# Kernel optimization log

Hardware: AMD Instinct MI355X
Metric: run time of the kernel (lower is better)

Reference implementation:

```python
import jax, jax.numpy as jnp
import numpy as np

B, S, V, E, R1, R2, L = 16, 128, 32000, 128, 256, 640, 512


def pos_encoding(seq_len, d, n=10000.0):
    # P[k, 2i] = sin(k / n^(2i/d)); P[k, 2i+1] = cos(k / n^(2i/d))
    k = jnp.arange(seq_len, dtype=jnp.float32)[:, None]
    i = jnp.arange(d // 2, dtype=jnp.float32)[None, :]
    ang = k / jnp.power(jnp.float32(n), 2.0 * i / d)
    P = jnp.zeros((seq_len, d), dtype=jnp.float32)
    P = P.at[:, 0::2].set(jnp.sin(ang)).at[:, 1::2].set(jnp.cos(ang))
    return P


def setup_inputs() -> dict:
    key = jax.random.key(0)
    ks = iter(jax.random.split(key, 40))

    def lin(fin, fout):
        W = jax.random.normal(next(ks), (fin, fout), jnp.float32) / np.sqrt(fin)
        b = jax.random.normal(next(ks), (fout,), jnp.float32) * 0.01
        return W, b

    inp = {}
    inp['x'] = jax.random.normal(next(ks), (B, S, V), jnp.float32)
    inp['W_emb'], inp['b_emb'] = lin(V, E)
    inp['W_pos1'], inp['b_pos1'] = lin(2 * E, E)
    inp['W_red'], inp['b_red'] = lin(S * E, R1)
    inp['W_pos2'], inp['b_pos2'] = lin(2 * R1, R1)
    inp['W_red2'], inp['b_red2'] = lin(S * R1, R2)
    inp['W_pos3'], inp['b_pos3'] = lin(2 * R2, R2)
    inp['W_down2'], inp['b_down2'] = lin(R2, L)
    inp['W_flat'], inp['b_flat'] = lin(L * S, L)
    inp['W_d1'], inp['b_d1'] = lin(L, L)
    inp['W_d2'], inp['b_d2'] = lin(L, L)
    inp['W_d3'], inp['b_d3'] = lin(L, L)
    inp['W_p1'], inp['b_p1'] = lin(L, V)
    inp['W_p2'], inp['b_p2'] = lin(L, V)
    return inp


def _square_memory(h):
    # einsum('bij,bkm->bikj') factorizes: out[b,i,k,j] = h[b,i,j] * sum_m h[b,k,m]
    b, s, d = h.shape
    row_sum = h.sum(axis=-1)                       # (B, S)
    q = h[:, :, None, :] * row_sum[:, None, :, None]  # (B, S, S, D)
    return q.reshape(b, s, s * d)


def reference(x, W_emb, b_emb, W_pos1, b_pos1, W_red, b_red, W_pos2, b_pos2,
              W_red2, b_red2, W_pos3, b_pos3, W_down2, b_down2, W_flat, b_flat,
              W_d1, b_d1, W_d2, b_d2, W_d3, b_d3, W_p1, b_p1, W_p2, b_p2):
    relu = jax.nn.relu
    h = relu(x @ W_emb + b_emb)                                  # (B,S,E)
    h = h + relu(pos_encoding(S, 2 * E) @ W_pos1 + b_pos1)
    h = relu(_square_memory(h) @ W_red + b_red)                  # (B,S,R1)
    h = h + relu(pos_encoding(S, 2 * R1) @ W_pos2 + b_pos2)
    h = relu(_square_memory(h) @ W_red2 + b_red2)                # (B,S,R2)
    h = h + relu(pos_encoding(S, 2 * R2) @ W_pos3 + b_pos3)
    h = relu(h @ W_down2 + b_down2)                              # (B,S,L)
    h = relu(h.reshape(h.shape[0], -1) @ W_flat + b_flat)        # (B,L)
    h = relu(h @ W_d1 + b_d1)
    p1 = h @ W_p1 + b_p1
    h = relu(h @ W_d2 + b_d2)
    p2 = h @ W_p2 + b_p2
    h = relu(h @ W_d3 + b_d3)
    p3 = h @ W_p1 + b_p1  # faithful to source: project_1 reused (project_3 unused)
    return p1 + p2 + p3
```

## Files before the change

### kernel.cpp

```cpp
#include <hip/hip_runtime.h>

typedef float  f4   __attribute__((ext_vector_type(4)));
typedef __bf16 bf8_t __attribute__((ext_vector_type(8)));
typedef __bf16 bf4_t __attribute__((ext_vector_type(4)));

__device__ __forceinline__ void glds16(const void* g, void* l) {
    __builtin_amdgcn_global_load_lds(
        (const __attribute__((address_space(1))) void*)g,
        (__attribute__((address_space(3))) void*)l, 16, 0, 0);
}

__global__ __launch_bounds__(256)
void prep_kernel(float* __restrict__ P1, float* __restrict__ P2,
                 float* __restrict__ P3,
                 const float* __restrict__ bp1, const float* __restrict__ bp2,
                 float* __restrict__ bc, float* __restrict__ rs2,
                 const float* __restrict__ Wemb, __bf16* __restrict__ WembT,
                 const float* __restrict__ Wd2, __bf16* __restrict__ Wd2T,
                 const float* __restrict__ Wq1, __bf16* __restrict__ Wq1T,
                 const float* __restrict__ Wq2, __bf16* __restrict__ Wq2T,
                 const float* __restrict__ Wq3, __bf16* __restrict__ Wq3T) {
    const int bid = blockIdx.x;
    const int t = threadIdx.x;
    if (bid < 5280) {
        const float* src; __bf16* dst; int CN, RK, tn, local;
        if (bid < 4000)      { src = Wemb; dst = WembT; RK = 32000; CN = 128; tn = 4;  local = bid; }
        else if (bid < 4320) { src = Wd2;  dst = Wd2T;  RK = 640;   CN = 512; tn = 16; local = bid - 4000; }
        else if (bid < 4352) { src = Wq1;  dst = Wq1T;  RK = 256;   CN = 128; tn = 4;  local = bid - 4320; }
        else if (bid < 4480) { src = Wq2;  dst = Wq2T;  RK = 512;   CN = 256; tn = 8;  local = bid - 4352; }
        else                 { src = Wq3;  dst = Wq3T;  RK = 1280;  CN = 640; tn = 20; local = bid - 4480; }
        const int kt = local / tn, ntl = local - kt * tn;
        const int k0 = kt * 32, n0 = ntl * 32;
        __shared__ float tile[32][33];
        const int r = t >> 3, c4 = (t & 7) * 4;
        const f4 v = *(const f4*)(src + (long)(k0 + r) * CN + n0 + c4);
        tile[r][c4] = v[0]; tile[r][c4 + 1] = v[1];
        tile[r][c4 + 2] = v[2]; tile[r][c4 + 3] = v[3];
        __syncthreads();
        bf4_t o2;
        o2[0] = (__bf16)tile[c4][r];     o2[1] = (__bf16)tile[c4 + 1][r];
        o2[2] = (__bf16)tile[c4 + 2][r]; o2[3] = (__bf16)tile[c4 + 3][r];
        *(bf4_t*)(dst + (long)(n0 + r) * RK + k0 + c4) = o2;
        return;
    }
    int idx = (bid - 5280) * 256 + t;
    const int n1 = 128 * 256, n2 = 128 * 512;
    const int nP = 262144;
    if (idx < nP) {
        float* P; int d, local;
        if (idx < n1)           { P = P1; d = 256;  local = idx; }
        else if (idx < n1 + n2) { P = P2; d = 512;  local = idx - n1; }
        else                    { P = P3; d = 1280; local = idx - n1 - n2; }
        int s = local / d;
        int k = local - s * d;
        int i = k >> 1;
        float ang = (float)s * powf(10000.0f, (-2.0f * (float)i) / (float)d);
        P[local] = (k & 1) ? cosf(ang) : sinf(ang);
    } else if (idx < nP + 32000) {
        int j = idx - nP;
        bc[j] = 2.f * bp1[j] + bp2[j];
    } else if (idx < nP + 32000 + 2048) {
        rs2[idx - nP - 32000] = 0.f;
    }
}

template<int BMODE>
__device__ __forceinline__ void gemm_dev(
    float* As0, float* As1, float* Bb0, float* Bb1,
    const float* __restrict__ A, const void* __restrict__ Bv,
    const void* __restrict__ B2v, float* __restrict__ C,
    const float* __restrict__ bias, const float* __restrict__ addsrc,
    float* __restrict__ rsum,
    int M, int N, int K, int lda, int ldb, int ldc, int kswitch,
    long sA, long sB, long sC, int ksplit, int kchunk, int relu,
    int bn, int bm, int bz) {

    const int t = threadIdx.x;
    const int batch = bz / ksplit;
    const int kz = bz - batch * ksplit;
    const int m0 = bm * 64, n0 = bn * 128;
    const int kb = kz * kchunk;
    const int ke = (kb + kchunk < K) ? (kb + kchunk) : K;
    const int nit = (ke - kb + 31) >> 5;

    const int lane = t & 63;
    const int w = t >> 6;
    const int wm = w >> 1, wn = w & 1;
    const int fr = lane & 15;
    const int fq = (lane >> 4) * 8;

    f4 acc[2][4];
#pragma unroll
    for (int mt = 0; mt < 2; ++mt)
#pragma unroll
        for (int nt = 0; nt < 4; ++nt) acc[mt][nt] = (f4){0.f, 0.f, 0.f, 0.f};

    const float* Ab = A + (long)batch * sA;
    const int mvalid = M - m0;

    const int ra = t >> 3;
    const int ja = (t & 7) ^ (ra & 7);
    const float* aS0 = Ab + (long)(m0 + ra) * lda + 4 * ja;
    const float* aS1 = aS0 + 32L * lda;

    const __bf16* bTS0 = nullptr; const __bf16* bTS1 = nullptr;
    const float* bNS0 = nullptr; const float* bNS2 = nullptr;
    if constexpr (BMODE == 0) {
        const __bf16* BT = (const __bf16*)Bv + (long)batch * sB;
        const int nb = t >> 2;
        const int fb = (nb & 3) ^ ((nb >> 2) & 3);
        const int jb = (t & 3) ^ fb;
        bTS0 = BT + (long)(n0 + nb) * ldb + 8 * jb;
        bTS1 = bTS0 + 64L * ldb;
    } else {
        const float* Bn = (const float*)Bv + (long)batch * sB;
        bNS0 = Bn + (long)(t >> 5) * ldb + n0 + (t & 31) * 4;
        const float* Bn2 = (const float*)(B2v ? B2v : Bv);
        bNS2 = Bn2 + (long)(t >> 5) * ldb + n0 + (t & 31) * 4;
    }

    auto STAGE = [&](float* Ad, float* Bd, int k0) {
        if (ra < mvalid)      glds16(aS0 + k0, Ad + 4 * t);
        if (ra + 32 < mvalid) glds16(aS1 + k0, Ad + 1024 + 4 * t);
        if constexpr (BMODE == 0) {
            glds16(bTS0 + k0, Bd + 4 * t);
            glds16(bTS1 + k0, Bd + 1024 + 4 * t);
        } else {
            const float* bp = (k0 < kswitch) ? (bNS0 + (long)k0 * ldb)
                                             : (bNS2 + (long)(k0 - kswitch) * ldb);
            glds16(bp,             Bd + 4 * t);
            glds16(bp + 8L * ldb,  Bd + 1024 + 4 * t);
            glds16(bp + 16L * ldb, Bd + 2048 + 4 * t);
            glds16(bp + 24L * ldb, Bd + 3072 + 4 * t);
        }
    };

    const int R0 = wm * 32 + fr, R1 = R0 + 16;
    const int jq = (lane >> 4) * 2;
    const int x7 = R0 & 7;
    const int aO00 = R0 * 8 + (jq ^ x7);
    const int aO01 = R0 * 8 + ((jq + 1) ^ x7);
    const int aO10 = R1 * 8 + (jq ^ x7);
    const int aO11 = R1 * 8 + ((jq + 1) ^ x7);
    int bOf[4];
    if constexpr (BMODE == 0) {
        const int fbc = (fr & 3) ^ ((fr >> 2) & 3);
        const int jb2 = (lane >> 4) ^ fbc;
#pragma unroll
        for (int nt = 0; nt < 4; ++nt)
            bOf[nt] = ((wn * 64 + nt * 16 + fr) * 4 + jb2) * 8;
    } else {
#pragma unroll
        for (int nt = 0; nt < 4; ++nt)
            bOf[nt] = wn * 64 + nt * 16 + fr;
    }

    STAGE(As0, Bb0, kb);
    __syncthreads();
    int cur = 0;
    for (int i = 0; i < nit; ++i) {
        float* Ac = cur ? As1 : As0;
        float* Bc = cur ? Bb1 : Bb0;
        if (i + 1 < nit) STAGE(cur ? As0 : As1, cur ? Bb0 : Bb1, kb + (i + 1) * 32);

        f4 x0 = *(const f4*)(Ac + aO00 * 4);
        f4 x1 = *(const f4*)(Ac + aO01 * 4);
        f4 x2 = *(const f4*)(Ac + aO10 * 4);
        f4 x3 = *(const f4*)(Ac + aO11 * 4);
        bf8_t af0, af1;
#pragma unroll
        for (int q = 0; q < 4; ++q) {
            af0[q] = (__bf16)x0[q]; af0[4 + q] = (__bf16)x1[q];
            af1[q] = (__bf16)x2[q]; af1[4 + q] = (__bf16)x3[q];
        }
#pragma unroll
        for (int nt = 0; nt < 4; ++nt) {
            bf8_t bv;
            if constexpr (BMODE == 0) {
                bv = *(const bf8_t*)((const __bf16*)Bc + bOf[nt]);
            } else {
                const float* bb = Bc + fq * 128 + bOf[nt];
#pragma unroll
                for (int d = 0; d < 8; ++d) bv[d] = (__bf16)bb[d * 128];
            }
            acc[0][nt] = __builtin_amdgcn_mfma_f32_16x16x32_bf16(af0, bv, acc[0][nt], 0, 0, 0);
            acc[1][nt] = __builtin_amdgcn_mfma_f32_16x16x32_bf16(af1, bv, acc[1][nt], 0, 0, 0);
        }
        __syncthreads();
        cur ^= 1;
    }

    float* Cp; long ldcp;
    const bool fin = (ksplit == 1);
    if (!fin) { Cp = C + (long)(batch * ksplit + kz) * M * N; ldcp = N; }
    else      { Cp = C + (long)batch * sC;                    ldcp = ldc; }

    const int rb = m0 + wm * 32 + (lane >> 4) * 4;
    const int cb_ = n0 + wn * 64 + fr;
    float rowpart[2][4] = {{0.f,0.f,0.f,0.f},{0.f,0.f,0.f,0.f}};
#pragma unroll
    for (int mt = 0; mt < 2; ++mt) {
#pragma unroll
        for (int nt = 0; nt < 4; ++nt) {
            const int c = cb_ + nt * 16;
            const float bvl = (fin && bias) ? bias[c] : 0.f;
#pragma unroll
            for (int v = 0; v < 4; ++v) {
                const int r = rb + mt * 16 + v;
                if (r < M) {
                    float val = acc[mt][nt][v] + bvl;
                    if (fin && relu) val = fmaxf(val, 0.f);
                    if (fin && addsrc) val += addsrc[(long)r * ldcp + c];
                    Cp[(long)r * ldcp + c] = val;
                    rowpart[mt][v] += val;
                }
            }
        }
    }
    if (rsum) {
#pragma unroll
        for (int mt = 0; mt < 2; ++mt) {
#pragma unroll
            for (int v = 0; v < 4; ++v) {
                float s = rowpart[mt][v];
                s += __shfl_xor(s, 1); s += __shfl_xor(s, 2);
                s += __shfl_xor(s, 4); s += __shfl_xor(s, 8);
                const int r = rb + mt * 16 + v;
                if (fr == 0 && r < M) atomicAdd(&rsum[(long)bz * M + r], s);
            }
        }
    }
}

template<int BMODE>
__global__ __launch_bounds__(256)
void gemm_v2(const float* A, const void* Bv, const void* B2v, float* C,
             const float* bias, const float* addsrc, float* rsum,
             int M, int N, int K, int lda, int ldb, int ldc, int kswitch,
             long sA, long sB, long sC, int ksplit, int kchunk, int relu) {
    __shared__ __align__(16) float AsF[2][2048];
    __shared__ __align__(16) float Bbuf[2][BMODE ? 4096 : 2048];
    gemm_dev<BMODE>(&AsF[0][0], &AsF[1][0], &Bbuf[0][0], &Bbuf[1][0],
                    A, Bv, B2v, C, bias, addsrc, rsum,
                    M, N, K, lda, ldb, ldc, kswitch, sA, sB, sC,
                    ksplit, kchunk, relu,
                    blockIdx.x, blockIdx.y, blockIdx.z);
}

__global__ __launch_bounds__(256)
void mega1_kernel(const float* __restrict__ x, const __bf16* __restrict__ WembT,
                  float* __restrict__ partG1,
                  const float* __restrict__ P1, const __bf16* __restrict__ Q1T,
                  float* __restrict__ Q1o, const float* __restrict__ bq1,
                  const float* __restrict__ P2, const __bf16* __restrict__ Q2T,
                  float* __restrict__ Q2o, const float* __restrict__ bq2,
                  const float* __restrict__ P3, const __bf16* __restrict__ Q3T,
                  float* __restrict__ Q3o, const float* __restrict__ bq3) {
    __shared__ __align__(16) float AsF[2][2048];
    __shared__ __align__(16) float Bbuf[2][2048];
    float* A0 = &AsF[0][0]; float* A1 = &AsF[1][0];
    float* B0 = &Bbuf[0][0]; float* B1 = &Bbuf[1][0];
    const int bid = blockIdx.x;
    if (bid < 1024) {
        const int xc = bid & 7, j = bid >> 3;
        const int bz = xc + ((j >> 5) << 3);
        const int bm = j & 31;
        gemm_dev<0>(A0, A1, B0, B1, x, WembT, nullptr, partG1,
                    nullptr, nullptr, nullptr,
                    2048, 128, 32000, 32000, 32000, 128, 32000,
                    0, 0, 0, 32, 1024, 0, 0, bm, bz);
    } else if (bid < 1026) {
        gemm_dev<0>(A0, A1, B0, B1, P1, Q1T, nullptr, Q1o,
                    bq1, nullptr, nullptr,
                    128, 128, 256, 256, 256, 128, 256,
                    0, 0, 0, 1, 256, 1, 0, bid - 1024, 0);
    } else if (bid < 1030) {
        const int l = bid - 1026;
        gemm_dev<0>(A0, A1, B0, B1, P2, Q2T, nullptr, Q2o,
                    bq2, nullptr, nullptr,
                    128, 256, 512, 512, 512, 256, 512,
                    0, 0, 0, 1, 512, 1, l & 1, l >> 1, 0);
    } else {
        const int l = bid - 1030;
        gemm_dev<0>(A0, A1, B0, B1, P3, Q3T, nullptr, Q3o,
                    bq3, nullptr, nullptr,
                    128, 640, 1280, 1280, 1280, 640, 1280,
                    0, 0, 0, 1, 1280, 1, l % 5, l / 5, 0);
    }
}

__global__ __launch_bounds__(256)
void reduce_splitk(const float* __restrict__ part, float* __restrict__ outp,
                   const float* __restrict__ bias, int MN, int N, int ksplit,
                   int relu) {
    int idx = blockIdx.x * 256 + threadIdx.x;
    if (idx >= MN) return;
    float s = 0.f;
    for (int z = 0; z < ksplit; ++z) s += part[(long)z * MN + idx];
    if (bias) s += bias[idx % N];
    if (relu) s = fmaxf(s, 0.f);
    outp[idx] = s;
}

__global__ __launch_bounds__(256)
void reduce_rs_kernel(const float* __restrict__ part, float* __restrict__ h1,
                      const float* __restrict__ bias, const float* __restrict__ Q1,
                      float* __restrict__ rs1, int ksplit) {
    const int t = threadIdx.x;
    const int idx = blockIdx.x * 256 + t;
    float s = 0.f;
    for (int z = 0; z < ksplit; ++z) s += part[(long)z * 262144 + idx];
    s += bias[idx & 127];
    s = fmaxf(s, 0.f);
    s += Q1[idx & 16383];
    h1[idx] = s;
    float r = s;
    for (int off = 32; off > 0; off >>= 1) r += __shfl_down(r, off, 64);
    __shared__ float p[4];
    const int w = t >> 6, lane = t & 63;
    if (lane == 0) p[w] = r;
    __syncthreads();
    if (t < 2) rs1[(blockIdx.x << 1) + t] = p[t * 2] + p[t * 2 + 1];
}

extern "C" void kernel_launch(void* const* d_in, const int* in_sizes, int n_in,
                              void* d_out, int out_size, void* d_ws, size_t ws_size,
                              hipStream_t stream) {
    const float* x       = (const float*)d_in[0];
    const float* W_emb   = (const float*)d_in[1];
    const float* b_emb   = (const float*)d_in[2];
    const float* W_pos1  = (const float*)d_in[3];
    const float* b_pos1  = (const float*)d_in[4];
    const float* W_red   = (const float*)d_in[5];
    const float* b_red   = (const float*)d_in[6];
    const float* W_pos2  = (const float*)d_in[7];
    const float* b_pos2  = (const float*)d_in[8];
    const float* W_red2  = (const float*)d_in[9];
    const float* b_red2  = (const float*)d_in[10];
    const float* W_pos3  = (const float*)d_in[11];
    const float* b_pos3  = (const float*)d_in[12];
    const float* W_down2 = (const float*)d_in[13];
    const float* b_down2 = (const float*)d_in[14];
    const float* W_flat  = (const float*)d_in[15];
    const float* b_flat  = (const float*)d_in[16];
    const float* W_d1    = (const float*)d_in[17];
    const float* b_d1    = (const float*)d_in[18];
    const float* W_d2    = (const float*)d_in[19];
    const float* b_d2    = (const float*)d_in[20];
    const float* W_d3    = (const float*)d_in[21];
    const float* b_d3    = (const float*)d_in[22];
    const float* W_p1    = (const float*)d_in[23];
    const float* b_p1    = (const float*)d_in[24];
    const float* W_p2    = (const float*)d_in[25];
    const float* b_p2    = (const float*)d_in[26];
    float* out = (float*)d_out;
    float* ws  = (float*)d_ws;

    size_t o = 0;
    auto alloc = [&](size_t n) { size_t p = o; o += (n + 63) & ~(size_t)63; return p; };
    const size_t oP1 = alloc(128 * 256);
    const size_t oP2 = alloc(128 * 512);
    const size_t oP3 = alloc(128 * 1280);
    const size_t oQ1 = alloc(128 * 128);
    const size_t oQ2 = alloc(128 * 256);
    const size_t oQ3 = alloc(128 * 640);
    const size_t oBC = alloc(32000);
    const size_t oH1 = alloc(2048 * 128);
    const size_t oRS1 = alloc(2048);
    const size_t oRS2 = alloc(2048);
    const size_t oH2 = alloc(2048 * 256);
    const size_t oH3 = alloc(2048 * 640);
    const size_t oH4 = alloc(2048 * 512);
    const size_t oH5 = alloc(16 * 512);
    const size_t oH6c = alloc(16 * 1024);
    const size_t oCat = alloc(16 * 1024);
    const size_t oM1 = alloc(16 * 32768);
    const size_t oM2 = alloc(16 * 163840);
    const size_t oWembT = alloc(2048000);
    const size_t oWd2T  = alloc(163840);
    const size_t oQ1T   = alloc(16384);
    const size_t oQ2T   = alloc(65536);
    const size_t oQ3T   = alloc(409600);
    const size_t oRegA = alloc(32u * 262144);
    const size_t oPartG1 = oRegA, oPartF = oRegA;
    (void)ws_size; (void)in_sizes; (void)n_in; (void)out_size;

    __bf16* WembT = (__bf16*)(ws + oWembT);
    __bf16* Wd2T  = (__bf16*)(ws + oWd2T);
    __bf16* Q1T   = (__bf16*)(ws + oQ1T);
    __bf16* Q2T   = (__bf16*)(ws + oQ2T);
    __bf16* Q3T   = (__bf16*)(ws + oQ3T);

    dim3 blk(256);

    prep_kernel<<<dim3(6437), blk, 0, stream>>>(
        ws + oP1, ws + oP2, ws + oP3, b_p1, b_p2, ws + oBC, ws + oRS2,
        W_emb, WembT, W_down2, Wd2T, W_pos1, Q1T, W_pos2, Q2T, W_pos3, Q3T);
    mega1_kernel<<<dim3(1040), blk, 0, stream>>>(
        x, WembT, ws + oPartG1,
        ws + oP1, Q1T, ws + oQ1, b_pos1,
        ws + oP2, Q2T, ws + oQ2, b_pos2,
        ws + oP3, Q3T, ws + oQ3, b_pos3);
    reduce_rs_kernel<<<dim3(1024), blk, 0, stream>>>(ws + oPartG1, ws + oH1,
                                                     b_emb, ws + oQ1, ws + oRS1, 32);
    gemm_v2<1><<<dim3(256, 1, 1), blk, 0, stream>>>(ws + oRS1, W_red, nullptr,
        ws + oM1, nullptr, nullptr, nullptr,
        16, 32768, 128, 128, 32768, 32768, 128, 0, 0, 0, 1, 128, 0);
    gemm_v2<1><<<dim3(2, 2, 16), blk, 0, stream>>>(ws + oH1, ws + oM1, nullptr,
        ws + oH2, b_red, ws + oQ2, ws + oRS2,
        128, 256, 128, 128, 256, 256, 128, 16384, 32768, 32768, 1, 128, 1);
    gemm_v2<1><<<dim3(1280, 1, 1), blk, 0, stream>>>(ws + oRS2, W_red2, nullptr,
        ws + oM2, nullptr, nullptr, nullptr,
        16, 163840, 128, 128, 163840, 163840, 128, 0, 0, 0, 1, 128, 0);
    gemm_v2<1><<<dim3(5, 2, 16), blk, 0, stream>>>(ws + oH2, ws + oM2, nullptr,
        ws + oH3, b_red2, ws + oQ3, nullptr,
        128, 640, 256, 256, 640, 640, 256, 32768, 163840, 81920, 1, 256, 1);
    gemm_v2<0><<<dim3(4, 32, 1), blk, 0, stream>>>(ws + oH3, Wd2T, nullptr,
        ws + oH4, b_down2, nullptr, nullptr,
        2048, 512, 640, 640, 640, 512, 640, 0, 0, 0, 1, 640, 1);
    gemm_v2<1><<<dim3(4, 1, 64), blk, 0, stream>>>(ws + oH4, W_flat, nullptr,
        ws + oPartF, nullptr, nullptr, nullptr,
        16, 512, 65536, 65536, 512, 512, 65536, 0, 0, 0, 64, 1024, 0);
    reduce_splitk<<<dim3(32), blk, 0, stream>>>(ws + oPartF, ws + oH5, b_flat,
                                                8192, 512, 64, 1);
    gemm_v2<1><<<dim3(4, 1, 1), blk, 0, stream>>>(ws + oH5, W_d1, nullptr,
        ws + oH6c, b_d1, nullptr, nullptr,
        16, 512, 512, 512, 512, 1024, 512, 0, 0, 0, 1, 512, 1);
    gemm_v2<1><<<dim3(4, 1, 1), blk, 0, stream>>>(ws + oH6c, W_d2, nullptr,
        ws + oCat + 512, b_d2, nullptr, nullptr,
        16, 512, 512, 1024, 512, 1024, 512, 0, 0, 0, 1, 512, 1);
    gemm_v2<1><<<dim3(4, 1, 1), blk, 0, stream>>>(ws + oCat + 512, W_d3, nullptr,
        ws + oCat, b_d3, ws + oH6c, nullptr,
        16, 512, 512, 1024, 512, 1024, 512, 0, 0, 0, 1, 512, 1);
    gemm_v2<1><<<dim3(250, 1, 1), blk, 0, stream>>>(ws + oCat, W_p1, W_p2,
        out, ws + oBC, nullptr, nullptr,
        16, 32000, 1024, 1024, 32000, 32000, 512, 0, 0, 0, 1, 1024, 0);
}
```

Before: 363.1 us.

## Use partial vmcnt waits to keep next stage's async loads in flight

Restructures the double-buffered GEMM main loop so the next tile's global-to-LDS loads are issued, then only the previous stage's loads are awaited via s_waitcnt vmcnt(N) before a raw s_barrier. The full __syncthreads drain of all outstanding loads is removed. A-tile row predicates are replaced by clamping out-of-range rows to the last valid row, so every thread issues a fixed count of loads and the vmcnt value is exact. This overlaps memory with MFMA compute but depends on the hand-counted load numbers being correct, and clamped rows produce garbage accumulator rows that must be masked at store.

```diff
diff --git a/kernel.cpp b/kernel.cpp
--- a/kernel.cpp
+++ b/kernel.cpp
@@ -8,6 +8,12 @@
     __builtin_amdgcn_global_load_lds(
         (const __attribute__((address_space(1))) void*)g,
         (__attribute__((address_space(3))) void*)l, 16, 0, 0);
+}
+
+template<int N>
+__device__ __forceinline__ void wait_vm() {
+    asm volatile("s_waitcnt vmcnt(%0)" :: "n"(N) : "memory");
+    __builtin_amdgcn_sched_barrier(0);
 }
 
 __global__ __launch_bounds__(256)
@@ -100,8 +106,10 @@
 
     const int ra = t >> 3;
     const int ja = (t & 7) ^ (ra & 7);
-    const float* aS0 = Ab + (long)(m0 + ra) * lda + 4 * ja;
-    const float* aS1 = aS0 + 32L * lda;
+    const int r0 = (ra < mvalid) ? ra : (mvalid - 1);
+    const int r1 = (ra + 32 < mvalid) ? (ra + 32) : (mvalid - 1);
+    const float* aS0 = Ab + (long)(m0 + r0) * lda + 4 * ja;
+    const float* aS1 = Ab + (long)(m0 + r1) * lda + 4 * ja;
 
     const __bf16* bTS0 = nullptr; const __bf16* bTS1 = nullptr;
     const float* bNS0 = nullptr; const float* bNS2 = nullptr;
@@ -120,8 +128,8 @@
     }
 
     auto STAGE = [&](float* Ad, float* Bd, int k0) {
-        if (ra < mvalid)      glds16(aS0 + k0, Ad + 4 * t);
-        if (ra + 32 < mvalid) glds16(aS1 + k0, Ad + 1024 + 4 * t);
+        glds16(aS0 + k0, Ad + 4 * t);
+        glds16(aS1 + k0, Ad + 1024 + 4 * t);
         if constexpr (BMODE == 0) {
             glds16(bTS0 + k0, Bd + 4 * t);
             glds16(bTS1 + k0, Bd + 1024 + 4 * t);
@@ -134,6 +142,7 @@
             glds16(bp + 24L * ldb, Bd + 3072 + 4 * t);
         }
     };
+    constexpr int LPS = (BMODE == 0) ? 4 : 6;
 
     const int R0 = wm * 32 + fr, R1 = R0 + 16;
     const int jq = (lane >> 4) * 2;
@@ -155,14 +164,7 @@
             bOf[nt] = wn * 64 + nt * 16 + fr;
     }
 
-    STAGE(As0, Bb0, kb);
-    __syncthreads();
-    int cur = 0;
-    for (int i = 0; i < nit; ++i) {
-        float* Ac = cur ? As1 : As0;
-        float* Bc = cur ? Bb1 : Bb0;
-        if (i + 1 < nit) STAGE(cur ? As0 : As1, cur ? Bb0 : Bb1, kb + (i + 1) * 32);
-
+    auto COMPUTE = [&](const float* Ac, const float* Bc) {
         f4 x0 = *(const f4*)(Ac + aO00 * 4);
         f4 x1 = *(const f4*)(Ac + aO01 * 4);
         f4 x2 = *(const f4*)(Ac + aO10 * 4);
@@ -186,9 +188,22 @@
             acc[0][nt] = __builtin_amdgcn_mfma_f32_16x16x32_bf16(af0, bv, acc[0][nt], 0, 0, 0);
             acc[1][nt] = __builtin_amdgcn_mfma_f32_16x16x32_bf16(af1, bv, acc[1][nt], 0, 0, 0);
         }
-        __syncthreads();
+    };
+
+    STAGE(As0, Bb0, kb);
+    int cur = 0;
+    for (int i = 0; i < nit - 1; ++i) {
+        STAGE(cur ? As0 : As1, cur ? Bb0 : Bb1, kb + (i + 1) * 32);
+        wait_vm<LPS>();
+        __builtin_amdgcn_s_barrier();
+        COMPUTE(cur ? As1 : As0, cur ? Bb1 : Bb0);
+        __builtin_amdgcn_s_barrier();
+        __builtin_amdgcn_sched_barrier(0);
         cur ^= 1;
     }
+    wait_vm<0>();
+    __builtin_amdgcn_s_barrier();
+    COMPUTE(cur ? As1 : As0, cur ? Bb1 : Bb0);
 
     float* Cp; long ldcp;
     const bool fin = (ksplit == 1);
```

Measured after the change: 381.6 us. 5.1% more time.

## Fuse tail kernel chain into one cooperative persistent kernel with grid syncs

Applied to the files above, without the earlier changes.

Replaces the sequence of about a dozen small launches after mega1 (reduce, rank-1 GEMMs, down-projection, split-K flat, dense layers, output projection) with a single cooperative kernel of 512 blocks. Stages are separated by grid.sync instead of kernel boundaries. The aim is to remove per-launch overhead and the idle gaps between many tiny kernels. In exchange, occupancy is capped at 2 blocks per CU by launch bounds, large stages loop over tiles inside fewer blocks, and each grid barrier has its own cost.

```diff
diff --git a/kernel.cpp b/kernel.cpp
--- a/kernel.cpp
+++ b/kernel.cpp
@@ -1,4 +1,7 @@
 #include <hip/hip_runtime.h>
+#include <hip/hip_cooperative_groups.h>
+
+namespace cg = cooperative_groups;
 
 typedef float  f4   __attribute__((ext_vector_type(4)));
 typedef __bf16 bf8_t __attribute__((ext_vector_type(8)));
@@ -155,12 +158,13 @@
             bOf[nt] = wn * 64 + nt * 16 + fr;
     }
 
+    __syncthreads();
     STAGE(As0, Bb0, kb);
     __syncthreads();
     int cur = 0;
     for (int i = 0; i < nit; ++i) {
-        float* Ac = cur ? As1 : As0;
-        float* Bc = cur ? Bb1 : Bb0;
+        const float* Ac = cur ? As1 : As0;
+        const float* Bc = cur ? Bb1 : Bb0;
         if (i + 1 < nit) STAGE(cur ? As0 : As1, cur ? Bb0 : Bb1, kb + (i + 1) * 32);
 
         f4 x0 = *(const f4*)(Ac + aO00 * 4);
@@ -230,21 +234,6 @@
             }
         }
     }
-}
-
-template<int BMODE>
-__global__ __launch_bounds__(256)
-void gemm_v2(const float* A, const void* Bv, const void* B2v, float* C,
-             const float* bias, const float* addsrc, float* rsum,
-             int M, int N, int K, int lda, int ldb, int ldc, int kswitch,
-             long sA, long sB, long sC, int ksplit, int kchunk, int relu) {
-    __shared__ __align__(16) float AsF[2][2048];
-    __shared__ __align__(16) float Bbuf[2][BMODE ? 4096 : 2048];
-    gemm_dev<BMODE>(&AsF[0][0], &AsF[1][0], &Bbuf[0][0], &Bbuf[1][0],
-                    A, Bv, B2v, C, bias, addsrc, rsum,
-                    M, N, K, lda, ldb, ldc, kswitch, sA, sB, sC,
-                    ksplit, kchunk, relu,
-                    blockIdx.x, blockIdx.y, blockIdx.z);
 }
 
 __global__ __launch_bounds__(256)
@@ -289,38 +278,120 @@
     }
 }
 
-__global__ __launch_bounds__(256)
-void reduce_splitk(const float* __restrict__ part, float* __restrict__ outp,
-                   const float* __restrict__ bias, int MN, int N, int ksplit,
-                   int relu) {
-    int idx = blockIdx.x * 256 + threadIdx.x;
-    if (idx >= MN) return;
-    float s = 0.f;
-    for (int z = 0; z < ksplit; ++z) s += part[(long)z * MN + idx];
-    if (bias) s += bias[idx % N];
-    if (relu) s = fmaxf(s, 0.f);
-    outp[idx] = s;
-}
-
-__global__ __launch_bounds__(256)
-void reduce_rs_kernel(const float* __restrict__ part, float* __restrict__ h1,
-                      const float* __restrict__ bias, const float* __restrict__ Q1,
-                      float* __restrict__ rs1, int ksplit) {
+struct TailP {
+    const float* partG1; float* h1; const float* b_emb; const float* Q1; float* rs1;
+    const float* W_red; float* M1;
+    const float* h2w; float* h2; const float* b_red; const float* Q2; float* rs2;
+    const float* W_red2; float* M2;
+    float* h3; const float* b_red2; const float* Q3;
+    const __bf16* Wd2T; float* h4; const float* b_down2;
+    const float* W_flat; float* partF; float* h5; const float* b_flat;
+    const float* W_d1; const float* b_d1;
+    const float* W_d2; const float* b_d2;
+    const float* W_d3; const float* b_d3;
+    float* h6c; float* cat;
+    const float* W_p1; const float* W_p2; const float* bc; float* out;
+};
+
+__global__ __launch_bounds__(256, 2)
+void tail_kernel(TailP p) {
+    __shared__ __align__(16) float As[2][2048];
+    __shared__ __align__(16) float Bb[2][4096];
+    __shared__ float red4[4];
+    cg::grid_group grid = cg::this_grid();
+    const int bid = blockIdx.x;
     const int t = threadIdx.x;
-    const int idx = blockIdx.x * 256 + t;
-    float s = 0.f;
-    for (int z = 0; z < ksplit; ++z) s += part[(long)z * 262144 + idx];
-    s += bias[idx & 127];
-    s = fmaxf(s, 0.f);
-    s += Q1[idx & 16383];
-    h1[idx] = s;
-    float r = s;
-    for (int off = 32; off > 0; off >>= 1) r += __shfl_down(r, off, 64);
-    __shared__ float p[4];
-    const int w = t >> 6, lane = t & 63;
-    if (lane == 0) p[w] = r;
-    __syncthreads();
-    if (t < 2) rs1[(blockIdx.x << 1) + t] = p[t * 2] + p[t * 2 + 1];
+    float* A0 = &As[0][0]; float* A1 = &As[1][0];
+    float* B0 = &Bb[0][0]; float* B1 = &Bb[1][0];
+    const int GRID = 512;
+
+    for (int tile = bid; tile < 1024; tile += GRID) {
+        const int idx = tile * 256 + t;
+        float s = 0.f;
+        for (int z = 0; z < 32; ++z) s += p.partG1[(long)z * 262144 + idx];
+        s += p.b_emb[idx & 127];
+        s = fmaxf(s, 0.f);
+        s += p.Q1[idx & 16383];
+        p.h1[idx] = s;
+        float r = s;
+        for (int off = 32; off > 0; off >>= 1) r += __shfl_down(r, off, 64);
+        const int w = t >> 6, lane = t & 63;
+        if (lane == 0) red4[w] = r;
+        __syncthreads();
+        if (t < 2) p.rs1[(tile << 1) + t] = red4[t * 2] + red4[t * 2 + 1];
+        __syncthreads();
+    }
+    grid.sync();
+    if (bid < 256)
+        gemm_dev<1>(A0, A1, B0, B1, p.rs1, p.W_red, nullptr, p.M1,
+                    nullptr, nullptr, nullptr,
+                    16, 32768, 128, 128, 32768, 32768, 1 << 30,
+                    0, 0, 0, 1, 128, 0, bid, 0, 0);
+    grid.sync();
+    if (bid < 64)
+        gemm_dev<1>(A0, A1, B0, B1, p.h2w, p.M1, nullptr, p.h2,
+                    p.b_red, p.Q2, p.rs2,
+                    128, 256, 128, 128, 256, 256, 1 << 30,
+                    16384, 32768, 32768, 1, 128, 1,
+                    bid & 1, (bid >> 1) & 1, bid >> 2);
+    grid.sync();
+    for (int tile = bid; tile < 1280; tile += GRID)
+        gemm_dev<1>(A0, A1, B0, B1, p.rs2, p.W_red2, nullptr, p.M2,
+                    nullptr, nullptr, nullptr,
+                    16, 163840, 128, 128, 163840, 163840, 1 << 30,
+                    0, 0, 0, 1, 128, 0, tile, 0, 0);
+    grid.sync();
+    if (bid < 160) {
+        const int bn = bid % 5, rem = bid / 5;
+        gemm_dev<1>(A0, A1, B0, B1, p.h2, p.M2, nullptr, p.h3,
+                    p.b_red2, p.Q3, nullptr,
+                    128, 640, 256, 256, 640, 640, 1 << 30,
+                    32768, 163840, 81920, 1, 256, 1, bn, rem & 1, rem >> 1);
+    }
+    grid.sync();
+    if (bid < 128)
+        gemm_dev<0>(A0, A1, B0, B1, p.h3, p.Wd2T, nullptr, p.h4,
+                    p.b_down2, nullptr, nullptr,
+                    2048, 512, 640, 640, 640, 512, 1 << 30,
+                    0, 0, 0, 1, 640, 1, bid & 3, bid >> 2, 0);
+    grid.sync();
+    if (bid < 256)
+        gemm_dev<1>(A0, A1, B0, B1, p.h4, p.W_flat, nullptr, p.partF,
+                    nullptr, nullptr, nullptr,
+                    16, 512, 65536, 65536, 512, 512, 1 << 30,
+                    0, 0, 0, 64, 1024, 0, bid & 3, 0, bid >> 2);
+    grid.sync();
+    if (bid < 32) {
+        const int idx = bid * 256 + t;
+        float s = 0.f;
+        for (int z = 0; z < 64; ++z) s += p.partF[(long)z * 8192 + idx];
+        s += p.b_flat[idx & 511];
+        p.h5[idx] = fmaxf(s, 0.f);
+    }
+    grid.sync();
+    if (bid < 4)
+        gemm_dev<1>(A0, A1, B0, B1, p.h5, p.W_d1, nullptr, p.h6c,
+                    p.b_d1, nullptr, nullptr,
+                    16, 512, 512, 512, 512, 1024, 1 << 30,
+                    0, 0, 0, 1, 512, 1, bid, 0, 0);
+    grid.sync();
+    if (bid < 4)
+        gemm_dev<1>(A0, A1, B0, B1, p.h6c, p.W_d2, nullptr, p.cat + 512,
+                    p.b_d2, nullptr, nullptr,
+                    16, 512, 512, 1024, 512, 1024, 1 << 30,
+                    0, 0, 0, 1, 512, 1, bid, 0, 0);
+    grid.sync();
+    if (bid < 4)
+        gemm_dev<1>(A0, A1, B0, B1, p.cat + 512, p.W_d3, nullptr, p.cat,
+                    p.b_d3, p.h6c, nullptr,
+                    16, 512, 512, 1024, 512, 1024, 1 << 30,
+                    0, 0, 0, 1, 512, 1, bid, 0, 0);
+    grid.sync();
+    if (bid < 250)
+        gemm_dev<1>(A0, A1, B0, B1, p.cat, p.W_p1, p.W_p2, p.out,
+                    p.bc, nullptr, nullptr,
+                    16, 32000, 1024, 1024, 32000, 32000, 512,
+                    0, 0, 0, 1, 1024, 0, bid, 0, 0);
 }
 
 extern "C" void kernel_launch(void* const* d_in, const int* in_sizes, int n_in,
@@ -401,38 +472,22 @@
         ws + oP1, Q1T, ws + oQ1, b_pos1,
         ws + oP2, Q2T, ws + oQ2, b_pos2,
         ws + oP3, Q3T, ws + oQ3, b_pos3);
-    reduce_rs_kernel<<<dim3(1024), blk, 0, stream>>>(ws + oPartG1, ws + oH1,
-                                                     b_emb, ws + oQ1, ws + oRS1, 32);
-    gemm_v2<1><<<dim3(256, 1, 1), blk, 0, stream>>>(ws + oRS1, W_red, nullptr,
-        ws + oM1, nullptr, nullptr, nullptr,
-        16, 32768, 128, 128, 32768, 32768, 128, 0, 0, 0, 1, 128, 0);
-    gemm_v2<1><<<dim3(2, 2, 16), blk, 0, stream>>>(ws + oH1, ws + oM1, nullptr,
-        ws + oH2, b_red, ws + oQ2, ws + oRS2,
-        128, 256, 128, 128, 256, 256, 128, 16384, 32768, 32768, 1, 128, 1);
-    gemm_v2<1><<<dim3(1280, 1, 1), blk, 0, stream>>>(ws + oRS2, W_red2, nullptr,
-        ws + oM2, nullptr, nullptr, nullptr,
-        16, 163840, 128, 128, 163840, 163840, 128, 0, 0, 0, 1, 128, 0);
-    gemm_v2<1><<<dim3(5, 2, 16), blk, 0, stream>>>(ws + oH2, ws + oM2, nullptr,
-        ws + oH3, b_red2, ws + oQ3, nullptr,
-        128, 640, 256, 256, 640, 640, 256, 32768, 163840, 81920, 1, 256, 1);
-    gemm_v2<0><<<dim3(4, 32, 1), blk, 0, stream>>>(ws + oH3, Wd2T, nullptr,
-        ws + oH4, b_down2, nullptr, nullptr,
-        2048, 512, 640, 640, 640, 512, 640, 0, 0, 0, 1, 640, 1);
-    gemm_v2<1><<<dim3(4, 1, 64), blk, 0, stream>>>(ws + oH4, W_flat, nullptr,
-        ws + oPartF, nullptr, nullptr, nullptr,
-        16, 512, 65536, 65536, 512, 512, 65536, 0, 0, 0, 64, 1024, 0);
-    reduce_splitk<<<dim3(32), blk, 0, stream>>>(ws + oPartF, ws + oH5, b_flat,
-                                                8192, 512, 64, 1);
-    gemm_v2<1><<<dim3(4, 1, 1), blk, 0, stream>>>(ws + oH5, W_d1, nullptr,
-        ws + oH6c, b_d1, nullptr, nullptr,
-        16, 512, 512, 512, 512, 1024, 512, 0, 0, 0, 1, 512, 1);
-    gemm_v2<1><<<dim3(4, 1, 1), blk, 0, stream>>>(ws + oH6c, W_d2, nullptr,
-        ws + oCat + 512, b_d2, nullptr, nullptr,
-        16, 512, 512, 1024, 512, 1024, 512, 0, 0, 0, 1, 512, 1);
-    gemm_v2<1><<<dim3(4, 1, 1), blk, 0, stream>>>(ws + oCat + 512, W_d3, nullptr,
-        ws + oCat, b_d3, ws + oH6c, nullptr,
-        16, 512, 512, 1024, 512, 1024, 512, 0, 0, 0, 1, 512, 1);
-    gemm_v2<1><<<dim3(250, 1, 1), blk, 0, stream>>>(ws + oCat, W_p1, W_p2,
-        out, ws + oBC, nullptr, nullptr,
-        16, 32000, 1024, 1024, 32000, 32000, 512, 0, 0, 0, 1, 1024, 0);
-}
+    TailP tp;
+    tp.partG1 = ws + oPartG1; tp.h1 = ws + oH1; tp.b_emb = b_emb;
+    tp.Q1 = ws + oQ1; tp.rs1 = ws + oRS1;
+    tp.W_red = W_red; tp.M1 = ws + oM1;
+    tp.h2w = ws + oH1; tp.h2 = ws + oH2; tp.b_red = b_red;
+    tp.Q2 = ws + oQ2; tp.rs2 = ws + oRS2;
+    tp.W_red2 = W_red2; tp.M2 = ws + oM2;
+    tp.h3 = ws + oH3; tp.b_red2 = b_red2; tp.Q3 = ws + oQ3;
+    tp.Wd2T = Wd2T; tp.h4 = ws + oH4; tp.b_down2 = b_down2;
+    tp.W_flat = W_flat; tp.partF = ws + oPartF; tp.h5 = ws + oH5;
+    tp.b_flat = b_flat;
+    tp.W_d1 = W_d1; tp.b_d1 = b_d1;
+    tp.W_d2 = W_d2; tp.b_d2 = b_d2;
+    tp.W_d3 = W_d3; tp.b_d3 = b_d3;
+    tp.h6c = ws + oH6c; tp.cat = ws + oCat;
+    tp.W_p1 = W_p1; tp.W_p2 = W_p2; tp.bc = ws + oBC; tp.out = out;
+    void* kargs[] = { &tp };
+    hipLaunchCooperativeKernel((void*)tail_kernel, dim3(512), blk, kargs, 0, stream);
+}
```

Result: slower. 891.2 us (+145.4%).

## Add multi-stage LDS pipeline with vmcnt waits to gemm_v2 kernels

Applied to the files above, without the earlier changes.

Generalises the GEMM device routine to a DEPTH-stage circular LDS buffer. For DEPTH of 3 or more it prefetches several K-tiles ahead and uses explicit s_waitcnt vmcnt with raw barriers in place of __syncthreads. A-row loads are clamped to a valid row so every thread issues the same number of loads per stage, which keeps the vmcnt accounting exact. Most standalone GEMM launches now use depth 3 or 4. This raises LDS use per block, which can lower occupancy, in exchange for hiding more global-load latency.

```diff
diff --git a/kernel.cpp b/kernel.cpp
--- a/kernel.cpp
+++ b/kernel.cpp
@@ -64,9 +64,9 @@
     }
 }
 
-template<int BMODE>
+template<int BMODE, int DEPTH>
 __device__ __forceinline__ void gemm_dev(
-    float* As0, float* As1, float* Bb0, float* Bb1,
+    float* AsB, float* BbB,
     const float* __restrict__ A, const void* __restrict__ Bv,
     const void* __restrict__ B2v, float* __restrict__ C,
     const float* __restrict__ bias, const float* __restrict__ addsrc,
@@ -75,6 +75,9 @@
     long sA, long sB, long sC, int ksplit, int kchunk, int relu,
     int bn, int bm, int bz) {
 
+    constexpr int BSZ = BMODE ? 4096 : 2048;
+    constexpr int LPS = BMODE ? 6 : 4;
+
     const int t = threadIdx.x;
     const int batch = bz / ksplit;
     const int kz = bz - batch * ksplit;
@@ -100,8 +103,13 @@
 
     const int ra = t >> 3;
     const int ja = (t & 7) ^ (ra & 7);
-    const float* aS0 = Ab + (long)(m0 + ra) * lda + 4 * ja;
-    const float* aS1 = aS0 + 32L * lda;
+    int ar0, ar1;
+    if constexpr (DEPTH >= 3) {
+        ar0 = (ra < mvalid) ? ra : (mvalid - 1);
+        ar1 = (ra + 32 < mvalid) ? (ra + 32) : (mvalid - 1);
+    } else { ar0 = ra; ar1 = ra + 32; }
+    const float* aS0 = Ab + (long)(m0 + ar0) * lda + 4 * ja;
+    const float* aS1 = Ab + (long)(m0 + ar1) * lda + 4 * ja;
 
     const __bf16* bTS0 = nullptr; const __bf16* bTS1 = nullptr;
     const float* bNS0 = nullptr; const float* bNS2 = nullptr;
@@ -119,9 +127,16 @@
         bNS2 = Bn2 + (long)(t >> 5) * ldb + n0 + (t & 31) * 4;
     }
 
-    auto STAGE = [&](float* Ad, float* Bd, int k0) {
-        if (ra < mvalid)      glds16(aS0 + k0, Ad + 4 * t);
-        if (ra + 32 < mvalid) glds16(aS1 + k0, Ad + 1024 + 4 * t);
+    auto STAGE = [&](int d, int k0) {
+        float* Ad = AsB + d * 2048;
+        float* Bd = BbB + d * BSZ;
+        if constexpr (DEPTH >= 3) {
+            glds16(aS0 + k0, Ad + 4 * t);
+            glds16(aS1 + k0, Ad + 1024 + 4 * t);
+        } else {
+            if (ra < mvalid)      glds16(aS0 + k0, Ad + 4 * t);
+            if (ra + 32 < mvalid) glds16(aS1 + k0, Ad + 1024 + 4 * t);
+        }
         if constexpr (BMODE == 0) {
             glds16(bTS0 + k0, Bd + 4 * t);
             glds16(bTS1 + k0, Bd + 1024 + 4 * t);
@@ -155,14 +170,9 @@
             bOf[nt] = wn * 64 + nt * 16 + fr;
     }
 
-    STAGE(As0, Bb0, kb);
-    __syncthreads();
-    int cur = 0;
-    for (int i = 0; i < nit; ++i) {
-        float* Ac = cur ? As1 : As0;
-        float* Bc = cur ? Bb1 : Bb0;
-        if (i + 1 < nit) STAGE(cur ? As0 : As1, cur ? Bb0 : Bb1, kb + (i + 1) * 32);
-
+    auto COMPUTE = [&](int d) {
+        const float* Ac = AsB + d * 2048;
+        const float* Bc = BbB + d * BSZ;
         f4 x0 = *(const f4*)(Ac + aO00 * 4);
         f4 x1 = *(const f4*)(Ac + aO01 * 4);
         f4 x2 = *(const f4*)(Ac + aO10 * 4);
@@ -181,13 +191,42 @@
             } else {
                 const float* bb = Bc + fq * 128 + bOf[nt];
 #pragma unroll
-                for (int d = 0; d < 8; ++d) bv[d] = (__bf16)bb[d * 128];
+                for (int d2 = 0; d2 < 8; ++d2) bv[d2] = (__bf16)bb[d2 * 128];
             }
             acc[0][nt] = __builtin_amdgcn_mfma_f32_16x16x32_bf16(af0, bv, acc[0][nt], 0, 0, 0);
             acc[1][nt] = __builtin_amdgcn_mfma_f32_16x16x32_bf16(af1, bv, acc[1][nt], 0, 0, 0);
         }
+    };
+
+    if constexpr (DEPTH == 2) {
+        STAGE(0, kb);
         __syncthreads();
-        cur ^= 1;
+        int cur = 0;
+        for (int i = 0; i < nit; ++i) {
+            if (i + 1 < nit) STAGE(cur ^ 1, kb + (i + 1) * 32);
+            COMPUTE(cur);
+            __syncthreads();
+            cur ^= 1;
+        }
+    } else {
+        const int npre = (nit < DEPTH) ? nit : (DEPTH - 1);
+        for (int s = 0; s < npre; ++s) STAGE(s, kb + s * 32);
+        int i = 0;
+        for (; i + (DEPTH - 1) < nit; ++i) {
+            STAGE((i + DEPTH - 1) % DEPTH, kb + (i + DEPTH - 1) * 32);
+            asm volatile("s_waitcnt vmcnt(%0)" :: "n"((DEPTH - 1) * LPS) : "memory");
+            __builtin_amdgcn_sched_barrier(0);
+            __builtin_amdgcn_s_barrier();
+            __builtin_amdgcn_sched_barrier(0);
+            COMPUTE(i % DEPTH);
+            __builtin_amdgcn_s_barrier();
+            __builtin_amdgcn_sched_barrier(0);
+        }
+        asm volatile("s_waitcnt vmcnt(0)" ::: "memory");
+        __builtin_amdgcn_sched_barrier(0);
+        __builtin_amdgcn_s_barrier();
+        __builtin_amdgcn_sched_barrier(0);
+        for (; i < nit; ++i) COMPUTE(i % DEPTH);
     }
 
     float* Cp; long ldcp;
@@ -232,19 +271,19 @@
     }
 }
 
-template<int BMODE>
+template<int BMODE, int DEPTH>
 __global__ __launch_bounds__(256)
 void gemm_v2(const float* A, const void* Bv, const void* B2v, float* C,
              const float* bias, const float* addsrc, float* rsum,
              int M, int N, int K, int lda, int ldb, int ldc, int kswitch,
              long sA, long sB, long sC, int ksplit, int kchunk, int relu) {
-    __shared__ __align__(16) float AsF[2][2048];
-    __shared__ __align__(16) float Bbuf[2][BMODE ? 4096 : 2048];
-    gemm_dev<BMODE>(&AsF[0][0], &AsF[1][0], &Bbuf[0][0], &Bbuf[1][0],
-                    A, Bv, B2v, C, bias, addsrc, rsum,
-                    M, N, K, lda, ldb, ldc, kswitch, sA, sB, sC,
-                    ksplit, kchunk, relu,
-                    blockIdx.x, blockIdx.y, blockIdx.z);
+    __shared__ __align__(16) float AsF[DEPTH][2048];
+    __shared__ __align__(16) float Bbuf[DEPTH][BMODE ? 4096 : 2048];
+    gemm_dev<BMODE, DEPTH>(&AsF[0][0], &Bbuf[0][0],
+                           A, Bv, B2v, C, bias, addsrc, rsum,
+                           M, N, K, lda, ldb, ldc, kswitch, sA, sB, sC,
+                           ksplit, kchunk, relu,
+                           blockIdx.x, blockIdx.y, blockIdx.z);
 }
 
 __global__ __launch_bounds__(256)
@@ -258,34 +297,34 @@
                   float* __restrict__ Q3o, const float* __restrict__ bq3) {
     __shared__ __align__(16) float AsF[2][2048];
     __shared__ __align__(16) float Bbuf[2][2048];
-    float* A0 = &AsF[0][0]; float* A1 = &AsF[1][0];
-    float* B0 = &Bbuf[0][0]; float* B1 = &Bbuf[1][0];
+    float* A0 = &AsF[0][0];
+    float* B0 = &Bbuf[0][0];
     const int bid = blockIdx.x;
     if (bid < 1024) {
         const int xc = bid & 7, j = bid >> 3;
         const int bz = xc + ((j >> 5) << 3);
         const int bm = j & 31;
-        gemm_dev<0>(A0, A1, B0, B1, x, WembT, nullptr, partG1,
-                    nullptr, nullptr, nullptr,
-                    2048, 128, 32000, 32000, 32000, 128, 32000,
-                    0, 0, 0, 32, 1024, 0, 0, bm, bz);
+        gemm_dev<0, 2>(A0, B0, x, WembT, nullptr, partG1,
+                       nullptr, nullptr, nullptr,
+                       2048, 128, 32000, 32000, 32000, 128, 32000,
+                       0, 0, 0, 32, 1024, 0, 0, bm, bz);
     } else if (bid < 1026) {
-        gemm_dev<0>(A0, A1, B0, B1, P1, Q1T, nullptr, Q1o,
-                    bq1, nullptr, nullptr,
-                    128, 128, 256, 256, 256, 128, 256,
-                    0, 0, 0, 1, 256, 1, 0, bid - 1024, 0);
+        gemm_dev<0, 2>(A0, B0, P1, Q1T, nullptr, Q1o,
+                       bq1, nullptr, nullptr,
+                       128, 128, 256, 256, 256, 128, 256,
+                       0, 0, 0, 1, 256, 1, 0, bid - 1024, 0);
     } else if (bid < 1030) {
         const int l = bid - 1026;
-        gemm_dev<0>(A0, A1, B0, B1, P2, Q2T, nullptr, Q2o,
-                    bq2, nullptr, nullptr,
-                    128, 256, 512, 512, 512, 256, 512,
-                    0, 0, 0, 1, 512, 1, l & 1, l >> 1, 0);
+        gemm_dev<0, 2>(A0, B0, P2, Q2T, nullptr, Q2o,
+                       bq2, nullptr, nullptr,
+                       128, 256, 512, 512, 512, 256, 512,
+                       0, 0, 0, 1, 512, 1, l & 1, l >> 1, 0);
     } else {
         const int l = bid - 1030;
-        gemm_dev<0>(A0, A1, B0, B1, P3, Q3T, nullptr, Q3o,
-                    bq3, nullptr, nullptr,
-                    128, 640, 1280, 1280, 1280, 640, 1280,
-                    0, 0, 0, 1, 1280, 1, l % 5, l / 5, 0);
+        gemm_dev<0, 2>(A0, B0, P3, Q3T, nullptr, Q3o,
+                       bq3, nullptr, nullptr,
+                       128, 640, 1280, 1280, 1280, 640, 1280,
+                       0, 0, 0, 1, 1280, 1, l % 5, l / 5, 0);
     }
 }
 
@@ -337,10 +376,10 @@
     const float* b_pos2  = (const float*)d_in[8];
     const float* W_red2  = (const float*)d_in[9];
     const float* b_red2  = (const float*)d_in[10];
+    const float* W_down2 = (const float*)d_in[13];
+    const float* b_down2 = (const float*)d_in[14];
     const float* W_pos3  = (const float*)d_in[11];
     const float* b_pos3  = (const float*)d_in[12];
-    const float* W_down2 = (const float*)d_in[13];
-    const float* b_down2 = (const float*)d_in[14];
     const float* W_flat  = (const float*)d_in[15];
     const float* b_flat  = (const float*)d_in[16];
     const float* W_d1    = (const float*)d_in[17];
@@ -403,36 +442,36 @@
         ws + oP3, Q3T, ws + oQ3, b_pos3);
     reduce_rs_kernel<<<dim3(1024), blk, 0, stream>>>(ws + oPartG1, ws + oH1,
                                                      b_emb, ws + oQ1, ws + oRS1, 32);
-    gemm_v2<1><<<dim3(256, 1, 1), blk, 0, stream>>>(ws + oRS1, W_red, nullptr,
+    gemm_v2<1, 4><<<dim3(256, 1, 1), blk, 0, stream>>>(ws + oRS1, W_red, nullptr,
         ws + oM1, nullptr, nullptr, nullptr,
-        16, 32768, 128, 128, 32768, 32768, 128, 0, 0, 0, 1, 128, 0);
-    gemm_v2<1><<<dim3(2, 2, 16), blk, 0, stream>>>(ws + oH1, ws + oM1, nullptr,
+        16, 32768, 128, 128, 32768, 32768, 1 << 30, 0, 0, 0, 1, 128, 0);
+    gemm_v2<1, 4><<<dim3(2, 2, 16), blk, 0, stream>>>(ws + oH1, ws + oM1, nullptr,
         ws + oH2, b_red, ws + oQ2, ws + oRS2,
-        128, 256, 128, 128, 256, 256, 128, 16384, 32768, 32768, 1, 128, 1);
-    gemm_v2<1><<<dim3(1280, 1, 1), blk, 0, stream>>>(ws + oRS2, W_red2, nullptr,
+        128, 256, 128, 128, 256, 256, 1 << 30, 16384, 32768, 32768, 1, 128, 1);
+    gemm_v2<1, 3><<<dim3(1280, 1, 1), blk, 0, stream>>>(ws + oRS2, W_red2, nullptr,
         ws + oM2, nullptr, nullptr, nullptr,
-        16, 163840, 128, 128, 163840, 163840, 128, 0, 0, 0, 1, 128, 0);
-    gemm_v2<1><<<dim3(5, 2, 16), blk, 0, stream>>>(ws + oH2, ws + oM2, nullptr,
+        16, 163840, 128, 128, 163840, 163840, 1 << 30, 0, 0, 0, 1, 128, 0);
+    gemm_v2<1, 4><<<dim3(5, 2, 16), blk, 0, stream>>>(ws + oH2, ws + oM2, nullptr,
         ws + oH3, b_red2, ws + oQ3, nullptr,
-        128, 640, 256, 256, 640, 640, 256, 32768, 163840, 81920, 1, 256, 1);
-    gemm_v2<0><<<dim3(4, 32, 1), blk, 0, stream>>>(ws + oH3, Wd2T, nullptr,
+        128, 640, 256, 256, 640, 640, 1 << 30, 32768, 163840, 81920, 1, 256, 1);
+    gemm_v2<0, 4><<<dim3(4, 32, 1), blk, 0, stream>>>(ws + oH3, Wd2T, nullptr,
         ws + oH4, b_down2, nullptr, nullptr,
-        2048, 512, 640, 640, 640, 512, 640, 0, 0, 0, 1, 640, 1);
-    gemm_v2<1><<<dim3(4, 1, 64), blk, 0, stream>>>(ws + oH4, W_flat, nullptr,
+        2048, 512, 640, 640, 640, 512, 1 << 30, 0, 0, 0, 1, 640, 1);
+    gemm_v2<1, 4><<<dim3(4, 1, 64), blk, 0, stream>>>(ws + oH4, W_flat, nullptr,
         ws + oPartF, nullptr, nullptr, nullptr,
-        16, 512, 65536, 65536, 512, 512, 65536, 0, 0, 0, 64, 1024, 0);
+        16, 512, 65536, 65536, 512, 512, 1 << 30, 0, 0, 0, 64, 1024, 0);
     reduce_splitk<<<dim3(32), blk, 0, stream>>>(ws + oPartF, ws + oH5, b_flat,
                                                 8192, 512, 64, 1);
-    gemm_v2<1><<<dim3(4, 1, 1), blk, 0, stream>>>(ws + oH5, W_d1, nullptr,
+    gemm_v2<1, 4><<<dim3(4, 1, 1), blk, 0, stream>>>(ws + oH5, W_d1, nullptr,
         ws + oH6c, b_d1, nullptr, nullptr,
-        16, 512, 512, 512, 512, 1024, 512, 0, 0, 0, 1, 512, 1);
-    gemm_v2<1><<<dim3(4, 1, 1), blk, 0, stream>>>(ws + oH6c, W_d2, nullptr,
+        16, 512, 512, 512, 512, 1024, 1 << 30, 0, 0, 0, 1, 512, 1);
+    gemm_v2<1, 4><<<dim3(4, 1, 1), blk, 0, stream>>>(ws + oH6c, W_d2, nullptr,
         ws + oCat + 512, b_d2, nullptr, nullptr,
-        16, 512, 512, 1024, 512, 1024, 512, 0, 0, 0, 1, 512, 1);
-    gemm_v2<1><<<dim3(4, 1, 1), blk, 0, stream>>>(ws + oCat + 512, W_d3, nullptr,
+        16, 512, 512, 1024, 512, 1024, 1 << 30, 0, 0, 0, 1, 512, 1);
+    gemm_v2<1, 4><<<dim3(4, 1, 1), blk, 0, stream>>>(ws + oCat + 512, W_d3, nullptr,
         ws + oCat, b_d3, ws + oH6c, nullptr,
-        16, 512, 512, 1024, 512, 1024, 512, 0, 0, 0, 1, 512, 1);
-    gemm_v2<1><<<dim3(250, 1, 1), blk, 0, stream>>>(ws + oCat, W_p1, W_p2,
+        16, 512, 512, 1024, 512, 1024, 1 << 30, 0, 0, 0, 1, 512, 1);
+    gemm_v2<1, 4><<<dim3(250, 1, 1), blk, 0, stream>>>(ws + oCat, W_p1, W_p2,
         out, ws + oBC, nullptr, nullptr,
         16, 32000, 1024, 1024, 32000, 32000, 512, 0, 0, 0, 1, 1024, 0);
 }
```

Result: slower. 390.0 us (+7.4%).
